# Kernel optimization log

Hardware: AMD Instinct MI355X
Metric: run time of the kernel (lower is better)

## Reference

```python
import jax, jax.numpy as jnp
import numpy as np


def _dconv(x, W, b, d):
    # dilated 3x3 conv, padding=d so spatial size is preserved (NCHW / OIHW)
    y = jax.lax.conv_general_dilated(
        x, W, window_strides=(1, 1), padding=((d, d), (d, d)),
        rhs_dilation=(d, d), dimension_numbers=('NCHW', 'OIHW', 'NCHW'))
    return y + b[None, :, None, None]


def setup_inputs() -> dict:
    key = jax.random.key(0)
    ks = jax.random.split(key, 12)
    B, C, H, W = 2, 512, 64, 64
    s = 0.02  # keep pre-softmax energies in a sane range
    inp = {
        'x':  jax.random.normal(ks[0], (B, C, H, W), jnp.float32),
        'W1': jax.random.normal(ks[1], (128, 512, 3, 3), jnp.float32) * s,
        'b1': jnp.zeros((128,), jnp.float32),
        'W2': jax.random.normal(ks[2], (128, 512, 3, 3), jnp.float32) * s,
        'b2': jnp.zeros((128,), jnp.float32),
        'W3': jax.random.normal(ks[3], (128, 512, 3, 3), jnp.float32) * s,
        'b3': jnp.zeros((128,), jnp.float32),
        'W4': jax.random.normal(ks[4], (128, 512, 3, 3), jnp.float32) * s,
        'b4': jnp.zeros((128,), jnp.float32),
        'Wd':  jax.random.normal(ks[5], (512, 128), jnp.float32) * s,   # dense, 1x1 no bias
        'Wcc': jax.random.normal(ks[6], (256, 512), jnp.float32) * s,   # CCIFL conv 512->256
        'bcc': jnp.zeros((256,), jnp.float32),
        'Wd2': jax.random.normal(ks[7], (512, 256), jnp.float32) * s,   # dense2, 1x1 no bias
    }
    return inp


def reference(x, W1, b1, W2, b2, W3, b3, W4, b4, Wd, Wcc, bcc, Wd2):
    B, C, H, W = x.shape
    N = H * W
    # four dilated-conv feature maps, flattened to [B, 128, N]
    a1 = jax.nn.relu(_dconv(x, W1, b1, 2)).reshape(B, 128, N)
    a2 = jax.nn.relu(_dconv(x, W2, b2, 3)).reshape(B, 128, N)
    a3 = jax.nn.relu(_dconv(x, W3, b3, 5)).reshape(B, 128, N)
    a4 = jax.nn.relu(_dconv(x, W4, b4, 7)).reshape(B, 128, N)

    # spatial attention 1: softmax(a1^T a2), applied as a4 @ att
    att12 = jax.nn.softmax(jnp.einsum('bcn,bcm->bnm', a1, a2), axis=-1)
    o1 = jnp.einsum('bcn,bnm->bcm', a4, att12).reshape(B, 128, H, W)
    o1 = jnp.einsum('oc,bchw->bohw', Wd, o1)  # dense 128->512

    # spatial attention 2: softmax(a3^T a4), applied as a2 @ att
    att34 = jax.nn.softmax(jnp.einsum('bcn,bcm->bnm', a3, a4), axis=-1)
    o2 = jnp.einsum('bcn,bnm->bcm', a2, att34).reshape(B, 128, H, W)
    o2 = jnp.einsum('oc,bchw->bohw', Wd, o2)

    def ccifl(y):
        # GAP -> 1x1 conv (512->256) -> scalar qk attention (softmax over a 1x1 -> 1)
        g = jnp.mean(y, axis=(2, 3))                        # [B, 512]
        z = jnp.einsum('oc,bc->bo', Wcc, g) + bcc           # [B, 256]
        e = jnp.einsum('bc,bc->b', z, z)[:, None, None]     # [B, 1, 1]
        att = jax.nn.softmax(e, axis=-1)                    # == 1
        return z * att[:, 0, :]                             # [B, 256]

    c1 = jnp.einsum('oc,bc->bo', Wd2, ccifl(o1))            # [B, 512]
    c2 = jnp.einsum('oc,bc->bo', Wd2, ccifl(o2))
    # broadcast [B,512,1,1] channel attention over spatial dims + residual
    return c1[:, :, None, None] + c2[:, :, None, None] + x
```

## Files before the change

kernel.cpp:

```cpp
#include <hip/hip_runtime.h>
#include <hip/hip_bf16.h>

typedef short short8 __attribute__((ext_vector_type(8)));
typedef float f32x4 __attribute__((ext_vector_type(4)));
typedef unsigned short u16;

#define XT_OFF   0
#define XT_BYTES (2*78*78*512*2)
#define WR2_OFF  (XT_OFF + XT_BYTES)
#define WR2_BYTES (2*9*16*8*64*16)
#define AFTER_W  (WR2_OFF + WR2_BYTES)
#define P_OFF    AFTER_W
#define P_BYTES  (4*4*4096*128*2)
#define GA_OFF_P (P_OFF + P_BYTES)
#define CA_OFF   AFTER_W
#define CA_BYTES (4*4096*128*4)
#define GA_OFF_A (CA_OFF + CA_BYTES)
#define GA_BYTES 2048
#define GV_REL   GA_BYTES
#define ZV_REL   (GV_REL + 4*512*4)
#define CV_REL   (ZV_REL + 4*256*4)
#define TAIL_END (CV_REL + 2*512*4)
#define WS_NEED_P ((size_t)GA_OFF_P + TAIL_END)
#define WS_NEED_A ((size_t)GA_OFF_A + TAIL_END)

static __device__ __forceinline__ void async_cp16(u16* lds, const u16* g) {
  __builtin_amdgcn_global_load_lds(
      (const __attribute__((address_space(1))) void*)g,
      (__attribute__((address_space(3))) void*)lds, 16, 0, 0);
}

__global__ void zero_u4(uint4* __restrict__ p, int n) {
  int i = blockIdx.x * blockDim.x + threadIdx.x;
  int st = gridDim.x * blockDim.x;
  uint4 z = {0u, 0u, 0u, 0u};
  for (; i < n; i += st) p[i] = z;
}

__global__ void prep_misc(u16* __restrict__ xT,
                          const float* __restrict__ W2, const float* __restrict__ W4,
                          u16* __restrict__ Wr2, float* __restrict__ gapacc) {
  int bid = blockIdx.x;
  int t = threadIdx.x;
  if (bid < 288) {
    size_t off; int cnt;
    if (bid < 256) {
      int b = bid >> 7, rem = bid & 127, h = rem >> 1, side = rem & 1;
      off = ((size_t)(b * 78 + 7 + h) * 78 + (side ? 71 : 0)) * 512;
      cnt = 7 * 512;
    } else {
      int k = bid - 256;
      int b = k >> 4, topbot = (k >> 3) & 1, ch = k & 7;
      off = ((size_t)b * 78 + (topbot ? 71 : 0)) * 78 * 512 + (size_t)ch * 34944;
      cnt = 34944;
    }
    uint4* p = (uint4*)(xT + off);
    int n = cnt >> 3;
    uint4 z = {0u, 0u, 0u, 0u};
    for (int i = t; i < n; i += blockDim.x) p[i] = z;
  } else if (bid < 544) {
    int idx = bid - 288;
    int conv = idx >> 7, o = idx & 127;
    const float* W = conv ? W4 : W2;
    __shared__ float sw[4608];
    const float* src = W + (size_t)o * 4608;
    for (int k = 0; k < 18; ++k) sw[t + k * 256] = src[t + k * 256];
    __syncthreads();
    if (t < 144) {
      int tap = t >> 4, kc = t & 15;
      int wn = o >> 6, ni = (o >> 4) & 3;
      size_t base = (size_t)conv * 589824 + (size_t)(tap * 16 + kc) * 4096
                    + (wn * 4 + ni) * 512;
#pragma unroll
      for (int cg = 0; cg < 4; ++cg) {
        union { u16 h[8]; uint4 v; } pk;
#pragma unroll
        for (int e = 0; e < 8; ++e) {
          __hip_bfloat16 hb = __float2bfloat16(sw[(kc * 32 + cg * 8 + e) * 9 + tap]);
          pk.h[e] = *(u16*)&hb;
        }
        int lane = cg * 16 + (o & 15);
        *(uint4*)(Wr2 + base + lane * 8) = pk.v;
      }
    }
  } else {
    gapacc[t] = 0.f;
    gapacc[t + 256] = 0.f;
  }
}

__global__ void prep_x(const float* __restrict__ x, u16* __restrict__ xT) {
  __shared__ float tile[64][65];
  int bh = blockIdx.x >> 3, cc = blockIdx.x & 7;
  int b = bh >> 6, h = bh & 63;
  int t = threadIdx.x;
  int w = t & 63, cq4 = t >> 6;
  int pi = t >> 2, q = t & 3;
#pragma unroll
  for (int i = 0; i < 16; ++i) {
    int ci = cq4 + i * 4;
    tile[ci][w] = x[((b * 512 + cc * 64 + ci) * 4096) + h * 64 + w];
  }
  __syncthreads();
  union { u16 u[16]; uint4 v[2]; } pk;
#pragma unroll
  for (int k = 0; k < 16; ++k) {
    __hip_bfloat16 hb = __float2bfloat16(tile[q * 16 + k][pi]);
    pk.u[k] = *(u16*)&hb;
  }
  u16* dst = xT + ((size_t)(b * 78 + h + 7) * 78 + (pi + 7)) * 512 + cc * 64 + q * 16;
  *(uint4*)dst = pk.v[0];
  *(uint4*)(dst + 8) = pk.v[1];
}

template<int MODE>
__global__ __launch_bounds__(256, 2) void conv_mfma(
    const u16* __restrict__ xT, const u16* __restrict__ Wr2,
    u16* __restrict__ Pp, float* __restrict__ convacc) {
  __shared__ __align__(16) u16 Ab[2][8192];
  int bid = blockIdx.x;
  int xcd = bid & 7, j = bid >> 3, g = j >> 2, cq = j & 3;
  int u = g >> 2, pt = (g & 3) * 8 + xcd;
  int b = u & 1, conv = u >> 1;
  int d = conv ? 7 : 3;
  int h0 = pt * 2;
  const u16* xb = xT + (size_t)b * (78 * 78 * 512);
  int t = threadIdx.x, l = t & 63, wv = t >> 6;
  int wm = wv >> 1, wn = wv & 1;

  int slog = (l & 7) ^ (l >> 3);
  int wq = wv * 8 + (l >> 3);
  const u16* gA[4];
#pragma unroll
  for (int m = 0; m < 4; ++m) {
    int hh = m >> 1, mh = m & 1;
    gA[m] = xb + ((size_t)(h0 + hh - d + 7) * 78 + (mh * 32 + wq - d + 7)) * 512
            + cq * 128 + slog * 8;
  }
  const char* bB = (const char*)Wr2 + (size_t)conv * 1179648
                   + cq * 32768 + wn * 4096 + l * 16;

  int rbase = (wm * 64 + (l & 15)) * 64;
  int rs0 = (((l >> 4)) ^ (l & 7)) * 8;
  int rs1 = ((4 + (l >> 4)) ^ (l & 7)) * 8;

  f32x4 acc[4][4];
#pragma unroll
  for (int i = 0; i < 4; ++i)
#pragma unroll
    for (int jj = 0; jj < 4; ++jj) acc[i][jj] = (f32x4){0.f, 0.f, 0.f, 0.f};

  short8 bf0[2][4], bf1[2][4];

  auto issueA = [&](int buf) {
#pragma unroll
    for (int m = 0; m < 4; ++m)
      async_cp16(&Ab[buf][m * 2048 + wv * 512], gA[m]);
  };
  auto loadB = [&](short8 bf[2][4]) {
#pragma unroll
    for (int c01 = 0; c01 < 2; ++c01)
#pragma unroll
      for (int ni = 0; ni < 4; ++ni)
        bf[c01][ni] = *(const short8*)(bB + c01 * 8192 + ni * 1024);
  };
  auto advance = [&](int s) {
    int dA, dB;
    if (!(s & 1)) { dA = 64; dB = 16384; }
    else {
      dB = 114688;
      int tap = (s + 1) >> 1;
      dA = (tap % 3) ? (512 * d - 64) : (38912 * d - 64);
    }
#pragma unroll
    for (int m = 0; m < 4; ++m) gA[m] += dA;
    bB += dB;
  };
  auto compute = [&](int buf, short8 bf[2][4]) {
    const u16* A = Ab[buf];
    short8 af[2][4];
#pragma unroll
    for (int mi = 0; mi < 4; ++mi) {
      af[0][mi] = *(const short8*)&A[rbase + mi * 1024 + rs0];
      af[1][mi] = *(const short8*)&A[rbase + mi * 1024 + rs1];
    }
#pragma unroll
    for (int c01 = 0; c01 < 2; ++c01)
#pragma unroll
      for (int mi = 0; mi < 4; ++mi)
#pragma unroll
        for (int ni = 0; ni < 4; ++ni)
          acc[mi][ni] = __builtin_amdgcn_mfma_f32_16x16x32_bf16(
              af[c01][mi], bf[c01][ni], acc[mi][ni], 0, 0, 0);
  };

  issueA(0); loadB(bf0); advance(0);
  __syncthreads();
  for (int it = 0; it < 9; ++it) {
    int s = it * 2;
    issueA(1); loadB(bf1); advance(s + 1);
    compute(0, bf0);
    __syncthreads();
    if (it < 8) { issueA(0); loadB(bf0); advance(s + 2); }
    compute(1, bf1);
    __syncthreads();
  }

  if (MODE == 0) {
    u16* PP = Pp + ((size_t)(cq * 4 + u) * 4096 + pt * 128 + wm * 64 + (l >> 4) * 4) * 128
              + wn * 64 + (l & 15);
#pragma unroll
    for (int mi = 0; mi < 4; ++mi)
#pragma unroll
      for (int ni = 0; ni < 4; ++ni)
#pragma unroll
        for (int jj = 0; jj < 4; ++jj) {
          __hip_bfloat16 hv = __float2bfloat16(acc[mi][ni][jj]);
          PP[(mi * 16 + jj) * 128 + ni * 16] = *(u16*)&hv;
        }
  } else {
    float* ca = convacc + (size_t)u * 4096 * 128;
#pragma unroll
    for (int mi = 0; mi < 4; ++mi)
#pragma unroll
      for (int ni = 0; ni < 4; ++ni)
#pragma unroll
        for (int jj = 0; jj < 4; ++jj) {
          int pos = pt * 128 + wm * 64 + mi * 16 + (l >> 4) * 4 + jj;
          int oc = wn * 64 + ni * 16 + (l & 15);
          atomicAdd(&ca[pos * 128 + oc], acc[mi][ni][jj]);
        }
  }
}

__global__ void reduce_gap_p(const u16* __restrict__ P,
                             const float* __restrict__ b2, const float* __restrict__ b4,
                             float* __restrict__ gapacc) {
  int u = blockIdx.x >> 6, g = blockIdx.x & 63;
  int conv = u >> 1;
  const float* bias = conv ? b4 : b2;
  int t = threadIdx.x;
  int oct = (t & 15) * 8, pl = t >> 4;
  float bi[8];
  *(float4*)&bi[0] = *(const float4*)&bias[oct];
  *(float4*)&bi[4] = *(const float4*)&bias[oct + 4];
  float s[8];
#pragma unroll
  for (int e = 0; e < 8; ++e) s[e] = 0.f;
  for (int i = 0; i < 4; ++i) {
    int pos = g * 64 + pl * 4 + i;
    size_t base = ((size_t)u * 4096 + pos) * 128 + oct;
    float v[8];
#pragma unroll
    for (int e = 0; e < 8; ++e) v[e] = bi[e];
#pragma unroll
    for (int cq = 0; cq < 4; ++cq) {
      uint4 q = *(const uint4*)&P[base + (size_t)cq * 2097152];
      unsigned w[4] = {q.x, q.y, q.z, q.w};
#pragma unroll
      for (int k = 0; k < 4; ++k) {
        v[k * 2]     += __builtin_bit_cast(float, (w[k] & 0xffffu) << 16);
        v[k * 2 + 1] += __builtin_bit_cast(float, w[k] & 0xffff0000u);
      }
    }
#pragma unroll
    for (int e = 0; e < 8; ++e) s[e] += v[e] > 0.f ? v[e] : 0.f;
  }
  __shared__ float red[16][128];
#pragma unroll
  for (int e = 0; e < 8; ++e) red[pl][oct + e] = s[e];
  __syncthreads();
  if (t < 128) {
    float acc = 0.f;
#pragma unroll
    for (int r = 0; r < 16; ++r) acc += red[r][t];
    atomicAdd(&gapacc[u * 128 + t], acc);
  }
}

__global__ void reduce_gap_a(const float* __restrict__ convacc,
                             const float* __restrict__ b2, const float* __restrict__ b4,
                             float* __restrict__ gapacc) {
  int unit = blockIdx.x >> 5, chunk = blockIdx.x & 31;
  int conv = unit >> 1;
  const float* bias = conv ? b4 : b2;
  int t = threadIdx.x, oc = t & 127, half = t >> 7;
  const float* ca = convacc + (size_t)unit * 4096 * 128;
  float bi = bias[oc];
  float s = 0.f;
  for (int i = 0; i < 64; ++i) {
    int pos = chunk * 128 + half * 64 + i;
    float v = ca[pos * 128 + oc] + bi;
    s += v > 0.f ? v : 0.f;
  }
  __shared__ float red[2][128];
  red[half][oc] = s;
  __syncthreads();
  if (t < 128) atomicAdd(&gapacc[unit * 128 + t], red[0][t] + red[1][t]);
}

__global__ void dense1(const float* __restrict__ gapacc, const float* __restrict__ Wd,
                       float* __restrict__ gv) {
  int o = blockIdx.x, t = threadIdx.x;
  float w = Wd[o * 128 + t];
  float p0 = w * gapacc[2 * 128 + t];
  float p1 = w * gapacc[0 * 128 + t];
  float p2 = w * gapacc[3 * 128 + t];
  float p3 = w * gapacc[1 * 128 + t];
#pragma unroll
  for (int m = 1; m < 64; m <<= 1) {
    p0 += __shfl_xor(p0, m); p1 += __shfl_xor(p1, m);
    p2 += __shfl_xor(p2, m); p3 += __shfl_xor(p3, m);
  }
  __shared__ float red[2][4];
  if ((t & 63) == 0) {
    red[t >> 6][0] = p0; red[t >> 6][1] = p1;
    red[t >> 6][2] = p2; red[t >> 6][3] = p3;
  }
  __syncthreads();
  if (t < 4) {
    const float inv = 1.f / 4096.f;
    gv[t * 512 + o] = (red[0][t] + red[1][t]) * inv;
  }
}

__global__ void dense2(const float* __restrict__ gv, const float* __restrict__ Wcc,
                       const float* __restrict__ bcc, float* __restrict__ zv) {
  int o = blockIdx.x, t = threadIdx.x;
  float w0 = Wcc[o * 512 + t], w1 = Wcc[o * 512 + 256 + t];
  float p[4];
#pragma unroll
  for (int c = 0; c < 4; ++c)
    p[c] = w0 * gv[c * 512 + t] + w1 * gv[c * 512 + 256 + t];
#pragma unroll
  for (int m = 1; m < 64; m <<= 1)
#pragma unroll
    for (int c = 0; c < 4; ++c) p[c] += __shfl_xor(p[c], m);
  __shared__ float red[4][4];
  if ((t & 63) == 0)
#pragma unroll
    for (int c = 0; c < 4; ++c) red[t >> 6][c] = p[c];
  __syncthreads();
  if (t < 4) {
    float s = bcc[o];
#pragma unroll
    for (int wv = 0; wv < 4; ++wv) s += red[wv][t];
    zv[t * 256 + o] = s;
  }
}

__global__ void dense3(const float* __restrict__ zv, const float* __restrict__ Wd2,
                       float* __restrict__ cvec) {
  int o = blockIdx.x, t = threadIdx.x;
  float w = Wd2[o * 256 + t];
  float p0 = w * (zv[0 * 256 + t] + zv[1 * 256 + t]);
  float p1 = w * (zv[2 * 256 + t] + zv[3 * 256 + t]);
#pragma unroll
  for (int m = 1; m < 64; m <<= 1) {
    p0 += __shfl_xor(p0, m);
    p1 += __shfl_xor(p1, m);
  }
  __shared__ float red[4][2];
  if ((t & 63) == 0) { red[t >> 6][0] = p0; red[t >> 6][1] = p1; }
  __syncthreads();
  if (t < 2) {
    float s = red[0][t] + red[1][t] + red[2][t] + red[3][t];
    cvec[t * 512 + o] = s;
  }
}

__global__ void final_add(const float* __restrict__ x, const float* __restrict__ cvec,
                          float* __restrict__ out) {
  int i = blockIdx.x * blockDim.x + threadIdx.x;
  int st = gridDim.x * blockDim.x;
  const float4* x4 = (const float4*)x;
  float4* o4 = (float4*)out;
  for (; i < 1048576; i += st) {
    int flat = i << 2;
    int b = flat >> 21;
    int ch = (flat >> 12) & 511;
    float c = cvec[b * 512 + ch];
    float4 v = x4[i];
    v.x += c; v.y += c; v.z += c; v.w += c;
    o4[i] = v;
  }
}

extern "C" void kernel_launch(void* const* d_in, const int* in_sizes, int n_in,
                              void* d_out, int out_size, void* d_ws, size_t ws_size,
                              hipStream_t stream) {
  const float* x   = (const float*)d_in[0];
  const float* W2  = (const float*)d_in[3];
  const float* b2  = (const float*)d_in[4];
  const float* W4  = (const float*)d_in[7];
  const float* b4  = (const float*)d_in[8];
  const float* Wd  = (const float*)d_in[9];
  const float* Wcc = (const float*)d_in[10];
  const float* bcc = (const float*)d_in[11];
  const float* Wd2 = (const float*)d_in[12];
  float* out = (float*)d_out;

  char* ws = (char*)d_ws;
  u16* xT  = (u16*)(ws + XT_OFF);
  u16* Wr2 = (u16*)(ws + WR2_OFF);

  const bool partial = ws_size >= WS_NEED_P;
  size_t ga_off = partial ? GA_OFF_P : GA_OFF_A;
  float* gapacc = (float*)(ws + ga_off);
  float* gv     = (float*)(ws + ga_off + GV_REL);
  float* zv     = (float*)(ws + ga_off + ZV_REL);
  float* cvec   = (float*)(ws + ga_off + CV_REL);

  prep_misc<<<545, 256, 0, stream>>>(xT, W2, W4, Wr2, gapacc);
  prep_x<<<1024, 256, 0, stream>>>(x, xT);

  if (partial) {
    u16* Pp = (u16*)(ws + P_OFF);
    conv_mfma<0><<<512, 256, 0, stream>>>(xT, Wr2, Pp, nullptr);
    reduce_gap_p<<<256, 256, 0, stream>>>(Pp, b2, b4, gapacc);
  } else {
    float* convacc = (float*)(ws + CA_OFF);
    zero_u4<<<512, 256, 0, stream>>>((uint4*)convacc, CA_BYTES / 16);
    conv_mfma<1><<<512, 256, 0, stream>>>(xT, Wr2, nullptr, convacc);
    reduce_gap_a<<<128, 256, 0, stream>>>(convacc, b2, b4, gapacc);
  }

  dense1<<<512, 128, 0, stream>>>(gapacc, Wd, gv);
  dense2<<<256, 256, 0, stream>>>(gv, Wcc, bcc, zv);
  dense3<<<512, 256, 0, stream>>>(zv, Wd2, cvec);
  final_add<<<2048, 256, 0, stream>>>(x, cvec, out);
}
```

Baseline: 58.67 us.

## Merge prep kernels into one launch and use partial-vmcnt barriers in conv loop

The x transpose/bf16 pack kernel is folded into the misc prep kernel, so one launch covers transpose, halo zeroing, weight repacking and accumulator reset. This removes a kernel launch and the serialization gap between the two prep kernels. In the MFMA conv main loop, __syncthreads is replaced by a hand-built barrier that waits only for vmcnt(8) and is fenced with sched_barriers. The intent is that the async A-tile LDS loads are complete at the barrier while the eight register B loads stay in flight, overlapping them with the barrier. This relies on in-order vmcnt accounting and on the compiler not reordering memory operations around the fences.

```diff
diff --git a/kernel.cpp b/kernel.cpp
--- a/kernel.cpp
+++ b/kernel.cpp
@@ -37,19 +37,41 @@
   for (; i < n; i += st) p[i] = z;
 }
 
-__global__ void prep_misc(u16* __restrict__ xT,
-                          const float* __restrict__ W2, const float* __restrict__ W4,
-                          u16* __restrict__ Wr2, float* __restrict__ gapacc) {
+__global__ void prep_all(const float* __restrict__ x, u16* __restrict__ xT,
+                         const float* __restrict__ W2, const float* __restrict__ W4,
+                         u16* __restrict__ Wr2, float* __restrict__ gapacc) {
   int bid = blockIdx.x;
   int t = threadIdx.x;
-  if (bid < 288) {
+  if (bid < 1024) {
+    __shared__ float tile[64][65];
+    int bh = bid >> 3, cc = bid & 7;
+    int b = bh >> 6, h = bh & 63;
+    int w = t & 63, cq4 = t >> 6;
+    int pi = t >> 2, q = t & 3;
+#pragma unroll
+    for (int i = 0; i < 16; ++i) {
+      int ci = cq4 + i * 4;
+      tile[ci][w] = x[((b * 512 + cc * 64 + ci) * 4096) + h * 64 + w];
+    }
+    __syncthreads();
+    union { u16 u[16]; uint4 v[2]; } pk;
+#pragma unroll
+    for (int k = 0; k < 16; ++k) {
+      __hip_bfloat16 hb = __float2bfloat16(tile[q * 16 + k][pi]);
+      pk.u[k] = *(u16*)&hb;
+    }
+    u16* dst = xT + ((size_t)(b * 78 + h + 7) * 78 + (pi + 7)) * 512 + cc * 64 + q * 16;
+    *(uint4*)dst = pk.v[0];
+    *(uint4*)(dst + 8) = pk.v[1];
+  } else if (bid < 1312) {
+    int hb = bid - 1024;
     size_t off; int cnt;
-    if (bid < 256) {
-      int b = bid >> 7, rem = bid & 127, h = rem >> 1, side = rem & 1;
+    if (hb < 256) {
+      int b = hb >> 7, rem = hb & 127, h = rem >> 1, side = rem & 1;
       off = ((size_t)(b * 78 + 7 + h) * 78 + (side ? 71 : 0)) * 512;
       cnt = 7 * 512;
     } else {
-      int k = bid - 256;
+      int k = hb - 256;
       int b = k >> 4, topbot = (k >> 3) & 1, ch = k & 7;
       off = ((size_t)b * 78 + (topbot ? 71 : 0)) * 78 * 512 + (size_t)ch * 34944;
       cnt = 34944;
@@ -58,8 +80,8 @@
     int n = cnt >> 3;
     uint4 z = {0u, 0u, 0u, 0u};
     for (int i = t; i < n; i += blockDim.x) p[i] = z;
-  } else if (bid < 544) {
-    int idx = bid - 288;
+  } else if (bid < 1568) {
+    int idx = bid - 1312;
     int conv = idx >> 7, o = idx & 127;
     const float* W = conv ? W4 : W2;
     __shared__ float sw[4608];
@@ -87,30 +109,6 @@
     gapacc[t] = 0.f;
     gapacc[t + 256] = 0.f;
   }
-}
-
-__global__ void prep_x(const float* __restrict__ x, u16* __restrict__ xT) {
-  __shared__ float tile[64][65];
-  int bh = blockIdx.x >> 3, cc = blockIdx.x & 7;
-  int b = bh >> 6, h = bh & 63;
-  int t = threadIdx.x;
-  int w = t & 63, cq4 = t >> 6;
-  int pi = t >> 2, q = t & 3;
-#pragma unroll
-  for (int i = 0; i < 16; ++i) {
-    int ci = cq4 + i * 4;
-    tile[ci][w] = x[((b * 512 + cc * 64 + ci) * 4096) + h * 64 + w];
-  }
-  __syncthreads();
-  union { u16 u[16]; uint4 v[2]; } pk;
-#pragma unroll
-  for (int k = 0; k < 16; ++k) {
-    __hip_bfloat16 hb = __float2bfloat16(tile[q * 16 + k][pi]);
-    pk.u[k] = *(u16*)&hb;
-  }
-  u16* dst = xT + ((size_t)(b * 78 + h + 7) * 78 + (pi + 7)) * 512 + cc * 64 + q * 16;
-  *(uint4*)dst = pk.v[0];
-  *(uint4*)(dst + 8) = pk.v[1];
 }
 
 template<int MODE>
@@ -156,6 +154,7 @@
 #pragma unroll
     for (int m = 0; m < 4; ++m)
       async_cp16(&Ab[buf][m * 2048 + wv * 512], gA[m]);
+    __builtin_amdgcn_sched_barrier(0);
   };
   auto loadB = [&](short8 bf[2][4]) {
 #pragma unroll
@@ -163,6 +162,12 @@
 #pragma unroll
       for (int ni = 0; ni < 4; ++ni)
         bf[c01][ni] = *(const short8*)(bB + c01 * 8192 + ni * 1024);
+  };
+  auto cbar = [&]() {
+    __builtin_amdgcn_sched_barrier(0);
+    asm volatile("s_waitcnt vmcnt(8)" ::: "memory");
+    __builtin_amdgcn_s_barrier();
+    __builtin_amdgcn_sched_barrier(0);
   };
   auto advance = [&](int s) {
     int dA, dB;
@@ -195,15 +200,15 @@
   };
 
   issueA(0); loadB(bf0); advance(0);
-  __syncthreads();
+  cbar();
   for (int it = 0; it < 9; ++it) {
     int s = it * 2;
     issueA(1); loadB(bf1); advance(s + 1);
     compute(0, bf0);
-    __syncthreads();
+    cbar();
     if (it < 8) { issueA(0); loadB(bf0); advance(s + 2); }
     compute(1, bf1);
-    __syncthreads();
+    cbar();
   }
 
   if (MODE == 0) {
@@ -411,8 +416,7 @@
   float* zv     = (float*)(ws + ga_off + ZV_REL);
   float* cvec   = (float*)(ws + ga_off + CV_REL);
 
-  prep_misc<<<545, 256, 0, stream>>>(xT, W2, W4, Wr2, gapacc);
-  prep_x<<<1024, 256, 0, stream>>>(x, xT);
+  prep_all<<<1569, 256, 0, stream>>>(x, xT, W2, W4, Wr2, gapacc);
 
   if (partial) {
     u16* Pp = (u16*)(ws + P_OFF);
```

New measurement: 56.42 us. 1.04x faster.
